# Optimization experiments

Hardware: AMD Instinct MI355X
Metric: run time of the kernel (lower is better)

The kernel has to match this reference:

```python
import jax, jax.numpy as jnp
import numpy as np

D_MODEL = 1024
N_HEADS = 16
HEAD_DIM = D_MODEL // N_HEADS


def setup_inputs() -> dict:
    key = jax.random.key(0)
    ks = jax.random.split(key, 9)
    s = 0.02
    x = jax.random.normal(ks[0], (2, 2048, D_MODEL), dtype=jnp.float32)
    wq = jax.random.normal(ks[1], (D_MODEL, D_MODEL), dtype=jnp.float32) * s
    wk = jax.random.normal(ks[2], (D_MODEL, D_MODEL), dtype=jnp.float32) * s
    wv = jax.random.normal(ks[3], (D_MODEL, D_MODEL), dtype=jnp.float32) * s
    wo = jax.random.normal(ks[4], (D_MODEL, D_MODEL), dtype=jnp.float32) * s
    bq = jax.random.normal(ks[5], (D_MODEL,), dtype=jnp.float32) * s
    bk = jax.random.normal(ks[6], (D_MODEL,), dtype=jnp.float32) * s
    bv = jax.random.normal(ks[7], (D_MODEL,), dtype=jnp.float32) * s
    bo = jax.random.normal(ks[8], (D_MODEL,), dtype=jnp.float32) * s
    return {"x": x, "wq": wq, "bq": bq, "wk": wk, "bk": bk,
            "wv": wv, "bv": bv, "wo": wo, "bo": bo}


def reference(x, wq, bq, wk, bk, wv, bv, wo, bo):
    B, T, C = x.shape
    H, Dh = N_HEADS, HEAD_DIM
    # torch Linear: y = x @ W.T + b
    q = (x @ wq.T + bq).reshape(B, T, H, Dh).transpose(0, 2, 1, 3)  # [B,H,T,Dh]
    k = (x @ wk.T + bk).reshape(B, T, H, Dh).transpose(0, 2, 1, 3)
    v = (x @ wv.T + bv).reshape(B, T, H, Dh).transpose(0, 2, 1, 3)
    scale = 1.0 / jnp.sqrt(jnp.float32(Dh))
    score = jnp.einsum('bhqd,bhkd->bhqk', q, k) * scale  # [B,H,T,T]
    causal = jnp.triu(jnp.ones((T, T), dtype=jnp.bool_), k=1)
    score = jnp.where(causal[None, None], jnp.float32(-10000.0), score)
    attn = jax.nn.softmax(score, axis=-1)
    out = jnp.einsum('bhqk,bhkd->bhqd', attn, v)  # [B,H,T,Dh]
    out = out.transpose(0, 2, 1, 3).reshape(B, T, C)
    return out @ wo.T + bo
```

## Files before the change

kernel.cpp:

```cpp
#include <hip/hip_runtime.h>
#include <hip/hip_bf16.h>

typedef __bf16 bf16_t;
typedef __bf16 bf16x8 __attribute__((ext_vector_type(8)));
typedef __bf16 bf16x4 __attribute__((ext_vector_type(4)));
typedef float f32x4 __attribute__((ext_vector_type(4)));
typedef unsigned int u32;

#define D_MODEL 1024
#define T_SEQ   2048
#define N_HEADS 16

#define WAITVM(N) asm volatile("s_waitcnt vmcnt(" #N ")" ::: "memory")

__device__ __forceinline__ void gload_lds16(const void* g, void* l) {
  __builtin_amdgcn_global_load_lds((const __attribute__((address_space(1))) u32*)g,
                                   (__attribute__((address_space(3))) u32*)l, 16, 0, 0);
}

__device__ __forceinline__ float fast_exp2(float x) {
#if __has_builtin(__builtin_amdgcn_exp2f)
  return __builtin_amdgcn_exp2f(x);
#else
  return __expf(x * 0.69314718056f);
#endif
}

struct CastArgs { const float* src[5]; bf16_t* dst[5]; };

__global__ __launch_bounds__(256) void cast_all(CastArgs p) {
  unsigned i = (blockIdx.x * 256u + threadIdx.x) * 4u;
  int seg; unsigned off;
  if (i < 4194304u) { seg = 0; off = i; }
  else { unsigned r = i - 4194304u; seg = 1 + (int)(r >> 20); off = r & 1048575u; }
  const float4 v = *(const float4*)(p.src[seg] + off);
  bf16x4 o = { (bf16_t)v.x, (bf16_t)v.y, (bf16_t)v.z, (bf16_t)v.w };
  *(bf16x4*)(p.dst[seg] + off) = o;
}

#define QSCL 0.18033688011112042f

struct QKVArgs {
  const bf16_t* A;
  const bf16_t* W[3];
  const float* bias[3];
  bf16_t* out[3];
};

__global__ __launch_bounds__(512, 2) void qkv_gemm(QKVArgs p) {
  __shared__ bf16_t lds[2 * 28672];

  const int tid = threadIdx.x;
  const int l = tid & 63, wid = tid >> 6;
  const int lh = l >> 4, r15 = l & 15;

  const int lid = blockIdx.x;
  const int bx = lid >> 4, by = lid & 15;
  const int brow = bx * 256;
  const int gcol0 = by * 192;

  const int wr = (wid >> 2) * 128;
  const int wc = (wid & 3) * 48;
  const int wrc = (wr >> 4);
  const int wcc = (wc >> 4);
  const int sA = (lh ^ ((r15 >> 1) & 3)) * 8;
  const int roff = r15 * 32;

  const int srow = l >> 2;
  const int gs = ((l & 3) ^ ((l >> 3) & 3)) * 8;

  f32x4 acc[8][3];
  const f32x4 zero = {0.f, 0.f, 0.f, 0.f};
#pragma unroll
  for (int i = 0; i < 8; ++i)
#pragma unroll
    for (int j = 0; j < 3; ++j) acc[i][j] = zero;

  const bf16_t* A = p.A;

  auto stageA = [&](bf16_t* buf, int k0, int kh) {
#pragma unroll
    for (int i = 0; i < 2; ++i) {
      int c = wid * 2 + i;
      gload_lds16(A + (size_t)(brow + c * 16 + srow) * D_MODEL + k0 + kh * 32 + gs,
                  buf + kh * 8192 + c * 512);
    }
  };
  auto stageB = [&](bf16_t* buf, int k0) {
#pragma unroll
    for (int i = 0; i < 3; ++i) {
      int g = wid * 3 + i;
      int kh = g >= 12;
      int c = g - kh * 12;
      int gcol = gcol0 + c * 16 + srow;
      int z = gcol >> 10;
      const bf16_t* w = (z == 0) ? p.W[0] : ((z == 1) ? p.W[1] : p.W[2]);
      gload_lds16(w + (size_t)(gcol & 1023) * D_MODEL + k0 + kh * 32 + gs,
                  buf + 16384 + kh * 6144 + c * 512);
    }
  };

  stageA(lds, 0, 0);
  stageA(lds, 0, 1);
  stageB(lds, 0);
  WAITVM(0);
  __builtin_amdgcn_s_barrier();

  for (int t = 0; t < 16; ++t) {
    bf16_t* cur = lds + (t & 1) * 28672;
    bf16_t* nxt = lds + ((t + 1) & 1) * 28672;
    const int k1 = (t + 1) * 64;
    const bool more = (t < 15);

    bf16x8 bfr[3][2];
#pragma unroll
    for (int ph = 0; ph < 4; ++ph) {
      bf16x8 a[2][2];
#pragma unroll
      for (int jj = 0; jj < 2; ++jj)
#pragma unroll
        for (int kh = 0; kh < 2; ++kh)
          a[jj][kh] = *(const bf16x8*)(cur + kh * 8192 + (wrc + 2 * ph + jj) * 512 + roff + sA);
      if (ph == 0) {
#pragma unroll
        for (int ni = 0; ni < 3; ++ni)
#pragma unroll
          for (int kh = 0; kh < 2; ++kh)
            bfr[ni][kh] = *(const bf16x8*)(cur + 16384 + kh * 6144 + (wcc + ni) * 512 + roff + sA);
      }
      if (more) {
        if (ph == 0) stageA(nxt, k1, 0);
        else if (ph == 1) stageA(nxt, k1, 1);
        else if (ph == 2) stageB(nxt, k1);
      }
      __builtin_amdgcn_s_barrier();
      __builtin_amdgcn_s_setprio(1);
#pragma unroll
      for (int jj = 0; jj < 2; ++jj)
#pragma unroll
        for (int ni = 0; ni < 3; ++ni) {
          acc[2 * ph + jj][ni] = __builtin_amdgcn_mfma_f32_16x16x32_bf16(a[jj][0], bfr[ni][0], acc[2 * ph + jj][ni], 0, 0, 0);
          acc[2 * ph + jj][ni] = __builtin_amdgcn_mfma_f32_16x16x32_bf16(a[jj][1], bfr[ni][1], acc[2 * ph + jj][ni], 0, 0, 0);
        }
      __builtin_amdgcn_s_setprio(0);
      if (ph == 3 && more) WAITVM(0);
      __builtin_amdgcn_s_barrier();
    }
  }

#pragma unroll
  for (int ni = 0; ni < 3; ++ni) {
    const int col = gcol0 + wc + ni * 16 + r15;
    const int z = col >> 10;
    const int zc = col & 1023;
    const float* bias = (z == 0) ? p.bias[0] : ((z == 1) ? p.bias[1] : p.bias[2]);
    bf16_t* O = (z == 0) ? p.out[0] : ((z == 1) ? p.out[1] : p.out[2]);
    const float bz = bias[zc];
    if (z == 2) {
#pragma unroll
      for (int mi = 0; mi < 8; ++mi) {
        int row0 = brow + wr + mi * 16 + lh * 4;
        int bb = row0 >> 11, t0 = row0 & 2047;
        bf16x4 pk;
#pragma unroll
        for (int j = 0; j < 4; ++j) pk[j] = (bf16_t)(acc[mi][ni][j] + bz);
        *(bf16x4*)(O + (size_t)bb * (D_MODEL * T_SEQ) + (size_t)zc * T_SEQ + t0) = pk;
      }
    } else if (z == 0) {
#pragma unroll
      for (int mi = 0; mi < 8; ++mi) {
        int row0 = brow + wr + mi * 16 + lh * 4;
#pragma unroll
        for (int j = 0; j < 4; ++j)
          O[(size_t)(row0 + j) * D_MODEL + zc] = (bf16_t)((acc[mi][ni][j] + bz) * QSCL);
      }
    } else {
#pragma unroll
      for (int mi = 0; mi < 8; ++mi) {
        int row0 = brow + wr + mi * 16 + lh * 4;
#pragma unroll
        for (int j = 0; j < 4; ++j)
          O[(size_t)(row0 + j) * D_MODEL + zc] = (bf16_t)(acc[mi][ni][j] + bz);
      }
    }
  }
}

__device__ __forceinline__ void stage_ab64(
    const bf16_t* __restrict__ A, const bf16_t* __restrict__ W,
    bf16_t* buf, int brow, int bcol, int k0, int w, int l) {
  const int srow = l >> 2;
  const int scol = ((l & 3) ^ ((l >> 3) & 3)) * 8;
#pragma unroll
  for (int i = 0; i < 3; ++i) {
    int ch = w * 3 + i;
    const bf16_t* src = (ch < 4)
      ? A + (size_t)(brow + ch * 16 + srow) * D_MODEL + k0 + scol
      : W + (size_t)(bcol + (ch - 4) * 16 + srow) * D_MODEL + k0 + scol;
    gload_lds16(src, buf + ch * 512);
  }
}

__device__ __forceinline__ void gemm_tile_64(
    const bf16_t* __restrict__ A, const bf16_t* __restrict__ W,
    bf16_t* bufs, int brow, int bcol, f32x4 acc[2][4])
{
  const int tid = threadIdx.x;
  const int l = tid & 63, w = tid >> 6;
  const int wr = (w >> 1) * 32, wc = (w & 1) * 64;
  const int lh = l >> 4, r15 = l & 15;
  const int NS = D_MODEL / 32;

  stage_ab64(A, W, bufs + 0 * 6144, brow, bcol, 0, w, l);
  stage_ab64(A, W, bufs + 1 * 6144, brow, bcol, 32, w, l);

  for (int t = 0; t < NS; ++t) {
    bf16_t* bb = bufs + (t % 3) * 6144;
    if (t + 2 < NS) {
      stage_ab64(A, W, bufs + ((t + 2) % 3) * 6144, brow, bcol, (t + 2) * 32, w, l);
      WAITVM(6);
    } else if (t + 1 < NS) {
      WAITVM(3);
    } else {
      WAITVM(0);
    }
    __builtin_amdgcn_s_barrier();

    bf16x8 af[2], bfr[4];
#pragma unroll
    for (int mi = 0; mi < 2; ++mi) {
      int rr = wr + mi * 16 + r15;
      int s = lh ^ ((rr >> 1) & 3);
      af[mi] = *(const bf16x8*)(bb + rr * 32 + s * 8);
    }
#pragma unroll
    for (int ni = 0; ni < 4; ++ni) {
      int rr = wc + ni * 16 + r15;
      int s = lh ^ ((rr >> 1) & 3);
      bfr[ni] = *(const bf16x8*)(bb + 2048 + rr * 32 + s * 8);
    }
    __builtin_amdgcn_s_setprio(1);
#pragma unroll
    for (int mi = 0; mi < 2; ++mi)
#pragma unroll
      for (int ni = 0; ni < 4; ++ni)
        acc[mi][ni] = __builtin_amdgcn_mfma_f32_16x16x32_bf16(af[mi], bfr[ni], acc[mi][ni], 0, 0, 0);
    __builtin_amdgcn_s_setprio(0);
    __builtin_amdgcn_s_barrier();
  }
}

__global__ __launch_bounds__(256) void out_gemm(
    const bf16_t* __restrict__ A, const bf16_t* __restrict__ W,
    const float* __restrict__ bias, float* __restrict__ O)
{
  __shared__ bf16_t bufs[3 * 6144];
  f32x4 acc[2][4];
  f32x4 zero = {0.f, 0.f, 0.f, 0.f};
#pragma unroll
  for (int i = 0; i < 2; ++i)
#pragma unroll
    for (int j = 0; j < 4; ++j) acc[i][j] = zero;

  const int brow = blockIdx.x * 64, bcol = blockIdx.y * 128;
  gemm_tile_64(A, W, bufs, brow, bcol, acc);

  const int tid = threadIdx.x, l = tid & 63, w = tid >> 6;
  const int wr = (w >> 1) * 32, wc = (w & 1) * 64, lh = l >> 4, r15 = l & 15;
#pragma unroll
  for (int ni = 0; ni < 4; ++ni) {
    int col = bcol + wc + ni * 16 + r15;
    float bz = bias[col];
#pragma unroll
    for (int mi = 0; mi < 2; ++mi) {
      int row0 = brow + wr + mi * 16 + lh * 4;
#pragma unroll
      for (int j = 0; j < 4; ++j)
        O[(size_t)(row0 + j) * D_MODEL + col] = acc[mi][ni][j] + bz;
    }
  }
}

__device__ __forceinline__ void stage_k128(const bf16_t* Kg, bf16_t* Kd, int kv0, int w, int l) {
#pragma unroll
  for (int i = 0; i < 4; ++i) {
    int c = w * 4 + i;
    int row = c * 8 + (l >> 3);
    int gcol = ((l & 7) ^ ((l >> 3) & 7)) * 8;
    gload_lds16(Kg + (size_t)(kv0 + row) * D_MODEL + gcol, Kd + c * 512);
  }
}
__device__ __forceinline__ void stage_v128(const bf16_t* Vg, bf16_t* Vd, int kv0, int w, int l) {
#pragma unroll
  for (int i = 0; i < 4; ++i) {
    int c = w * 4 + i;
    int drow = c * 4 + (l >> 4);
    int gkv = ((l & 15) ^ (drow & 15)) * 8;
    gload_lds16(Vg + (size_t)drow * T_SEQ + kv0 + gkv, Vd + c * 512);
  }
}

__global__ __launch_bounds__(256) void flash_attn(
    const bf16_t* __restrict__ Qm, const bf16_t* __restrict__ Km,
    const bf16_t* __restrict__ Vtg, bf16_t* __restrict__ Om)
{
  __shared__ bf16_t Kls[128 * 64];
  __shared__ bf16_t Vls[64 * 128];
  __shared__ bf16_t Pls[4][2][16 * 72];

  const int tid = threadIdx.x, l = tid & 63, w = tid >> 6;
  const int lh = l >> 4, r15 = l & 15;

  const int lid = blockIdx.x;
  const int qt = 31 - (lid >> 5);
  const int bh = lid & 31;
  const int b = bh >> 4, h = bh & 15;
  const int nT = (qt >> 1) + 1;

  const size_t baseQ = (size_t)b * T_SEQ * D_MODEL + h * 64;
  const size_t baseVt = (size_t)b * (D_MODEL * T_SEQ) + (size_t)(h * 64) * T_SEQ;
  const bf16_t* Kg = Km + baseQ;
  const bf16_t* Vg = Vtg + baseVt;

  const int qw = qt * 64 + w * 16;
  const int qrow = qw + r15;

  bf16x8 qf[2];
  {
    const bf16_t* qp = Qm + baseQ + (size_t)(qw + r15) * D_MODEL + lh * 8;
    qf[0] = *(const bf16x8*)(qp);
    qf[1] = *(const bf16x8*)(qp + 32);
  }

  float l_r = 0.f;
  f32x4 o_acc[4];
  const f32x4 zero = {0.f, 0.f, 0.f, 0.f};
#pragma unroll
  for (int n = 0; n < 4; ++n) o_acc[n] = zero;

  bf16_t* PA = &Pls[w][0][0];
  bf16_t* PB = &Pls[w][1][0];

  stage_k128(Kg, Kls, 0, w, l);
  stage_v128(Vg, Vls, 0, w, l);
  WAITVM(0);
  __builtin_amdgcn_s_barrier();

  for (int t = 0; t < nT; ++t) {
    const int kv0 = t * 128;
    const bool more = (t + 1 < nT);
    const bool diag = (t == nT - 1);
    const bool skip2 = diag && ((qt & 1) == 0);

    f32x4 sf[8];
    auto qk_n = [&](int n) {
      const int kvc = n * 16 + r15;
      const int sw = kvc & 7;
      bf16x8 kf0 = *(const bf16x8*)(Kls + kvc * 64 + ((lh ^ sw) * 8));
      bf16x8 kf1 = *(const bf16x8*)(Kls + kvc * 64 + (((4 + lh) ^ sw) * 8));
      f32x4 a = zero;
      a = __builtin_amdgcn_mfma_f32_16x16x32_bf16(kf0, qf[0], a, 0, 0, 0);
      a = __builtin_amdgcn_mfma_f32_16x16x32_bf16(kf1, qf[1], a, 0, 0, 0);
      sf[n] = a;
    };
    __builtin_amdgcn_s_setprio(1);
#pragma unroll
    for (int n = 0; n < 4; ++n) qk_n(n);
    __builtin_amdgcn_s_setprio(0);
    if (!skip2) {
      __builtin_amdgcn_s_setprio(1);
#pragma unroll
      for (int n = 4; n < 8; ++n) qk_n(n);
      __builtin_amdgcn_s_setprio(0);
    }

    __builtin_amdgcn_s_barrier();
    if (more) stage_k128(Kg, Kls, kv0 + 128, w, l);

    auto sm_half = [&](int hh, bf16_t* P, bool dm) {
#pragma unroll
      for (int n2 = 0; n2 < 4; ++n2) {
        const int n = hh * 4 + n2;
        float pv[4];
#pragma unroll
        for (int j = 0; j < 4; ++j) {
          float pp = fast_exp2(sf[n][j]);
          if (dm) {
            const int kvcol = kv0 + hh * 64 + n2 * 16 + lh * 4 + j;
            if (kvcol > qrow) pp = 0.f;
          }
          pv[j] = pp;
          l_r += pp;
        }
        bf16x4 pk = { (bf16_t)pv[0], (bf16_t)pv[1], (bf16_t)pv[2], (bf16_t)pv[3] };
        *(bf16x4*)(P + r15 * 72 + (n2 * 2 + (lh >> 1)) * 8 + (lh & 1) * 4) = pk;
      }
    };
    sm_half(0, PA, diag);
    if (!skip2) sm_half(1, PB, diag);

    if (more) WAITVM(4); else WAITVM(0);

    auto pv_half = [&](int hh, const bf16_t* P) {
      bf16x8 pa0 = *(const bf16x8*)(P + r15 * 72 + lh * 8);
      bf16x8 pa1 = *(const bf16x8*)(P + r15 * 72 + (4 + lh) * 8);
      __builtin_amdgcn_s_setprio(1);
#pragma unroll
      for (int nD = 0; nD < 4; ++nD) {
        const int d = nD * 16 + r15;
        const int b0 = (hh * 8 + lh) ^ r15;
        const int b1 = (hh * 8 + 4 + lh) ^ r15;
        bf16x8 vf0 = *(const bf16x8*)(Vls + d * 128 + b0 * 8);
        bf16x8 vf1 = *(const bf16x8*)(Vls + d * 128 + b1 * 8);
        o_acc[nD] = __builtin_amdgcn_mfma_f32_16x16x32_bf16(vf0, pa0, o_acc[nD], 0, 0, 0);
        o_acc[nD] = __builtin_amdgcn_mfma_f32_16x16x32_bf16(vf1, pa1, o_acc[nD], 0, 0, 0);
      }
      __builtin_amdgcn_s_setprio(0);
    };
    pv_half(0, PA);
    if (!skip2) pv_half(1, PB);

    __builtin_amdgcn_s_barrier();
    if (more) {
      stage_v128(Vg, Vls, kv0 + 128, w, l);
      WAITVM(4);
    }
  }

  float ls = l_r;
  ls += __shfl_xor(ls, 16, 64);
  ls += __shfl_xor(ls, 32, 64);
  const float invl = 1.f / ls;
  bf16_t* orow = Om + (size_t)(b * T_SEQ + qw + r15) * D_MODEL + h * 64;
#pragma unroll
  for (int n = 0; n < 4; ++n) {
    bf16x4 pk = { (bf16_t)(o_acc[n][0] * invl), (bf16_t)(o_acc[n][1] * invl),
                  (bf16_t)(o_acc[n][2] * invl), (bf16_t)(o_acc[n][3] * invl) };
    *(bf16x4*)(orow + n * 16 + lh * 4) = pk;
  }
}

extern "C" void kernel_launch(void* const* d_in, const int* in_sizes, int n_in,
                              void* d_out, int out_size, void* d_ws, size_t ws_size,
                              hipStream_t stream) {
  const float* x  = (const float*)d_in[0];
  const float* wq = (const float*)d_in[1];
  const float* bq = (const float*)d_in[2];
  const float* wk = (const float*)d_in[3];
  const float* bk = (const float*)d_in[4];
  const float* wv = (const float*)d_in[5];
  const float* bv = (const float*)d_in[6];
  const float* wo = (const float*)d_in[7];
  const float* bo = (const float*)d_in[8];

  char* ws = (char*)d_ws;
  const size_t MB = 1024 * 1024;
  bf16_t* xb  = (bf16_t*)(ws);
  bf16_t* wqb = (bf16_t*)(ws + 8 * MB);
  bf16_t* wkb = (bf16_t*)(ws + 10 * MB);
  bf16_t* wvb = (bf16_t*)(ws + 12 * MB);
  bf16_t* wob = (bf16_t*)(ws + 14 * MB);
  bf16_t* qb  = (bf16_t*)(ws + 16 * MB);
  bf16_t* kb  = (bf16_t*)(ws + 24 * MB);
  bf16_t* vtb = (bf16_t*)(ws + 32 * MB);
  bf16_t* ob  = (bf16_t*)(ws + 40 * MB);

  CastArgs ca;
  ca.src[0] = x;  ca.dst[0] = xb;
  ca.src[1] = wq; ca.dst[1] = wqb;
  ca.src[2] = wk; ca.dst[2] = wkb;
  ca.src[3] = wv; ca.dst[3] = wvb;
  ca.src[4] = wo; ca.dst[4] = wob;
  cast_all<<<8192, 256, 0, stream>>>(ca);

  QKVArgs qa;
  qa.A = xb;
  qa.W[0] = wqb; qa.W[1] = wkb; qa.W[2] = wvb;
  qa.bias[0] = bq; qa.bias[1] = bk; qa.bias[2] = bv;
  qa.out[0] = qb; qa.out[1] = kb; qa.out[2] = vtb;
  qkv_gemm<<<256, 512, 0, stream>>>(qa);

  flash_attn<<<1024, 256, 0, stream>>>(qb, kb, vtb, ob);

  out_gemm<<<dim3(64, 8), 256, 0, stream>>>(ob, wob, bo, (float*)d_out);
}
```

Baseline: 94.70 us.

## Split long causal attention query tiles across two blocks with combine kernel

Query tiles 16-31 (the longest causal rows) now have their KV range split in half across two blocks. A lookup table orders the 1536 blocks so that long work is scheduled first. Each split block writes an unnormalised fp32 partial output and row sum to a workspace, and a new combine kernel adds the two partials, normalises and writes bf16. This targets the load imbalance and tail of the causal flash-attention grid, at the cost of extra global traffic and one more kernel launch. Summing partials without a max rescale is only valid because the existing kernel already uses no running max.

```diff
diff --git a/kernel.cpp b/kernel.cpp
--- a/kernel.cpp
+++ b/kernel.cpp
@@ -281,6 +281,17 @@
   }
 }
 
+__device__ const unsigned char SCHED[48] = {
+  62, 94, 63, 95, 92, 93, 15, 14,
+  60, 61, 58, 90, 59, 91, 88, 89, 13, 12,
+  56, 57, 54, 86, 55, 87, 84, 85, 11, 10,
+  52, 53, 50, 82, 51, 83, 80, 81, 9, 8,
+  48, 49, 7, 6,
+  5, 4,
+  3, 2,
+  1, 0
+};
+
 __device__ __forceinline__ void stage_k128(const bf16_t* Kg, bf16_t* Kd, int kv0, int w, int l) {
 #pragma unroll
   for (int i = 0; i < 4; ++i) {
@@ -302,7 +313,8 @@
 
 __global__ __launch_bounds__(256) void flash_attn(
     const bf16_t* __restrict__ Qm, const bf16_t* __restrict__ Km,
-    const bf16_t* __restrict__ Vtg, bf16_t* __restrict__ Om)
+    const bf16_t* __restrict__ Vtg, bf16_t* __restrict__ Om,
+    float* __restrict__ Pw)
 {
   __shared__ bf16_t Kls[128 * 64];
   __shared__ bf16_t Vls[64 * 128];
@@ -312,10 +324,17 @@
   const int lh = l >> 4, r15 = l & 15;
 
   const int lid = blockIdx.x;
-  const int qt = 31 - (lid >> 5);
+  const int e = SCHED[lid >> 5];
+  const int qt = e & 31;
+  const int mode = e >> 5;
   const int bh = lid & 31;
   const int b = bh >> 4, h = bh & 15;
   const int nT = (qt >> 1) + 1;
+  const int h0 = nT >> 1;
+  const int t0 = (mode == 2) ? h0 : 0;
+  const int t1 = (mode == 1) ? h0 : nT;
+  const bool split = (mode != 0);
+  const int s = (mode == 2) ? 1 : 0;
 
   const size_t baseQ = (size_t)b * T_SEQ * D_MODEL + h * 64;
   const size_t baseVt = (size_t)b * (D_MODEL * T_SEQ) + (size_t)(h * 64) * T_SEQ;
@@ -341,14 +360,14 @@
   bf16_t* PA = &Pls[w][0][0];
   bf16_t* PB = &Pls[w][1][0];
 
-  stage_k128(Kg, Kls, 0, w, l);
-  stage_v128(Vg, Vls, 0, w, l);
+  stage_k128(Kg, Kls, t0 * 128, w, l);
+  stage_v128(Vg, Vls, t0 * 128, w, l);
   WAITVM(0);
   __builtin_amdgcn_s_barrier();
 
-  for (int t = 0; t < nT; ++t) {
+  for (int t = t0; t < t1; ++t) {
     const int kv0 = t * 128;
-    const bool more = (t + 1 < nT);
+    const bool more = (t + 1 < t1);
     const bool diag = (t == nT - 1);
     const bool skip2 = diag && ((qt & 1) == 0);
 
@@ -430,13 +449,48 @@
   float ls = l_r;
   ls += __shfl_xor(ls, 16, 64);
   ls += __shfl_xor(ls, 32, 64);
-  const float invl = 1.f / ls;
-  bf16_t* orow = Om + (size_t)(b * T_SEQ + qw + r15) * D_MODEL + h * 64;
-#pragma unroll
-  for (int n = 0; n < 4; ++n) {
-    bf16x4 pk = { (bf16_t)(o_acc[n][0] * invl), (bf16_t)(o_acc[n][1] * invl),
-                  (bf16_t)(o_acc[n][2] * invl), (bf16_t)(o_acc[n][3] * invl) };
-    *(bf16x4*)(orow + n * 16 + lh * 4) = pk;
+
+  if (!split) {
+    const float invl = 1.f / ls;
+    bf16_t* orow = Om + (size_t)(b * T_SEQ + qw + r15) * D_MODEL + h * 64;
+#pragma unroll
+    for (int n = 0; n < 4; ++n) {
+      bf16x4 pk = { (bf16_t)(o_acc[n][0] * invl), (bf16_t)(o_acc[n][1] * invl),
+                    (bf16_t)(o_acc[n][2] * invl), (bf16_t)(o_acc[n][3] * invl) };
+      *(bf16x4*)(orow + n * 16 + lh * 4) = pk;
+    }
+  } else {
+    float* slot = Pw + ((size_t)((qt - 16) * 32 + bh) * 2 + s) * 4160;
+    float* prow = slot + (w * 16 + r15) * 64;
+#pragma unroll
+    for (int n = 0; n < 4; ++n)
+      *(f32x4*)(prow + n * 16 + lh * 4) = o_acc[n];
+    if (lh == 0) slot[4096 + w * 16 + r15] = ls;
+  }
+}
+
+__global__ __launch_bounds__(256) void combine_attn(
+    const float* __restrict__ Pw, bf16_t* __restrict__ Om)
+{
+  const int g = blockIdx.x;
+  const int qt = 16 + (g >> 5);
+  const int bh = g & 31;
+  const int b = bh >> 4, h = bh & 15;
+  const int row = threadIdx.x >> 2;
+  const int cs = (threadIdx.x & 3) * 16;
+
+  const float* s0 = Pw + (size_t)((qt - 16) * 32 + bh) * 2 * 4160;
+  const float* s1 = s0 + 4160;
+  const float invl = 1.f / (s0[4096 + row] + s1[4096 + row]);
+
+  bf16_t* orow = Om + (size_t)(b * T_SEQ + qt * 64 + row) * D_MODEL + h * 64 + cs;
+#pragma unroll
+  for (int k4 = 0; k4 < 4; ++k4) {
+    float4 a = *(const float4*)(s0 + row * 64 + cs + k4 * 4);
+    float4 c = *(const float4*)(s1 + row * 64 + cs + k4 * 4);
+    bf16x4 pk = { (bf16_t)((a.x + c.x) * invl), (bf16_t)((a.y + c.y) * invl),
+                  (bf16_t)((a.z + c.z) * invl), (bf16_t)((a.w + c.w) * invl) };
+    *(bf16x4*)(orow + k4 * 4) = pk;
   }
 }
 
@@ -464,6 +518,7 @@
   bf16_t* kb  = (bf16_t*)(ws + 24 * MB);
   bf16_t* vtb = (bf16_t*)(ws + 32 * MB);
   bf16_t* ob  = (bf16_t*)(ws + 40 * MB);
+  float* pbuf = (float*)(ws + 64 * MB);
 
   CastArgs ca;
   ca.src[0] = x;  ca.dst[0] = xb;
@@ -480,7 +535,8 @@
   qa.out[0] = qb; qa.out[1] = kb; qa.out[2] = vtb;
   qkv_gemm<<<256, 512, 0, stream>>>(qa);
 
-  flash_attn<<<1024, 256, 0, stream>>>(qb, kb, vtb, ob);
+  flash_attn<<<1536, 256, 0, stream>>>(qb, kb, vtb, ob, pbuf);
+  combine_attn<<<512, 256, 0, stream>>>(pbuf, ob);
 
   out_gemm<<<dim3(64, 8), 256, 0, stream>>>(ob, wob, bo, (float*)d_out);
 }
```

Result: slower. 102.2 us (+7.9%).

## Process two 64-row query tiles per flash-attention block to reuse staged K/V

Applied to the files above, without the earlier changes.

Each block now handles 128 query rows: each warp owns two 16-row groups, A and B, and each staged 128-wide K/V tile serves both groups. This halves the grid to 512 blocks and the number of K/V loads into LDS per query row. Block order is also interleaved so heavy and light causal tiles mix. The cost is more registers (two accumulator sets), a serialized A-then-B dependency through the shared P buffers, and a full vmcnt(0) wait each iteration instead of the earlier partial wait, which may reduce overlap and occupancy.

```diff
diff --git a/kernel.cpp b/kernel.cpp
--- a/kernel.cpp
+++ b/kernel.cpp
@@ -312,31 +312,37 @@
   const int lh = l >> 4, r15 = l & 15;
 
   const int lid = blockIdx.x;
-  const int qt = 31 - (lid >> 5);
+  const int g = lid >> 5;
+  const int qt = (g < 8) ? (15 - g) : (g - 8);
   const int bh = lid & 31;
   const int b = bh >> 4, h = bh & 15;
-  const int nT = (qt >> 1) + 1;
+  const int nT = qt + 1;
 
   const size_t baseQ = (size_t)b * T_SEQ * D_MODEL + h * 64;
   const size_t baseVt = (size_t)b * (D_MODEL * T_SEQ) + (size_t)(h * 64) * T_SEQ;
   const bf16_t* Kg = Km + baseQ;
   const bf16_t* Vg = Vtg + baseVt;
 
-  const int qw = qt * 64 + w * 16;
-  const int qrow = qw + r15;
-
-  bf16x8 qf[2];
+  const int qA = qt * 128 + w * 16;
+  const int qB = qA + 64;
+  const int qrowA = qA + r15;
+  const int qrowB = qB + r15;
+
+  bf16x8 qfA[2], qfB[2];
   {
-    const bf16_t* qp = Qm + baseQ + (size_t)(qw + r15) * D_MODEL + lh * 8;
-    qf[0] = *(const bf16x8*)(qp);
-    qf[1] = *(const bf16x8*)(qp + 32);
-  }
-
-  float l_r = 0.f;
-  f32x4 o_acc[4];
+    const bf16_t* qp = Qm + baseQ + (size_t)qrowA * D_MODEL + lh * 8;
+    qfA[0] = *(const bf16x8*)(qp);
+    qfA[1] = *(const bf16x8*)(qp + 32);
+    const bf16_t* qp2 = Qm + baseQ + (size_t)qrowB * D_MODEL + lh * 8;
+    qfB[0] = *(const bf16x8*)(qp2);
+    qfB[1] = *(const bf16x8*)(qp2 + 32);
+  }
+
+  float l_A = 0.f, l_B = 0.f;
+  f32x4 oA[4], oB[4];
   const f32x4 zero = {0.f, 0.f, 0.f, 0.f};
 #pragma unroll
-  for (int n = 0; n < 4; ++n) o_acc[n] = zero;
+  for (int n = 0; n < 4; ++n) { oA[n] = zero; oB[n] = zero; }
 
   bf16_t* PA = &Pls[w][0][0];
   bf16_t* PB = &Pls[w][1][0];
@@ -349,11 +355,9 @@
   for (int t = 0; t < nT; ++t) {
     const int kv0 = t * 128;
     const bool more = (t + 1 < nT);
-    const bool diag = (t == nT - 1);
-    const bool skip2 = diag && ((qt & 1) == 0);
-
-    f32x4 sf[8];
-    auto qk_n = [&](int n) {
+    const bool last = (t == nT - 1);
+
+    auto qk_n = [&](const bf16x8* qf, int n, f32x4* sf) {
       const int kvc = n * 16 + r15;
       const int sw = kvc & 7;
       bf16x8 kf0 = *(const bf16x8*)(Kls + kvc * 64 + ((lh ^ sw) * 8));
@@ -363,21 +367,7 @@
       a = __builtin_amdgcn_mfma_f32_16x16x32_bf16(kf1, qf[1], a, 0, 0, 0);
       sf[n] = a;
     };
-    __builtin_amdgcn_s_setprio(1);
-#pragma unroll
-    for (int n = 0; n < 4; ++n) qk_n(n);
-    __builtin_amdgcn_s_setprio(0);
-    if (!skip2) {
-      __builtin_amdgcn_s_setprio(1);
-#pragma unroll
-      for (int n = 4; n < 8; ++n) qk_n(n);
-      __builtin_amdgcn_s_setprio(0);
-    }
-
-    __builtin_amdgcn_s_barrier();
-    if (more) stage_k128(Kg, Kls, kv0 + 128, w, l);
-
-    auto sm_half = [&](int hh, bf16_t* P, bool dm) {
+    auto sm_half = [&](const f32x4* sf, int hh, bf16_t* P, int qrow, bool dm, float& lr) {
 #pragma unroll
       for (int n2 = 0; n2 < 4; ++n2) {
         const int n = hh * 4 + n2;
@@ -390,18 +380,13 @@
             if (kvcol > qrow) pp = 0.f;
           }
           pv[j] = pp;
-          l_r += pp;
+          lr += pp;
         }
         bf16x4 pk = { (bf16_t)pv[0], (bf16_t)pv[1], (bf16_t)pv[2], (bf16_t)pv[3] };
         *(bf16x4*)(P + r15 * 72 + (n2 * 2 + (lh >> 1)) * 8 + (lh & 1) * 4) = pk;
       }
     };
-    sm_half(0, PA, diag);
-    if (!skip2) sm_half(1, PB, diag);
-
-    if (more) WAITVM(4); else WAITVM(0);
-
-    auto pv_half = [&](int hh, const bf16_t* P) {
+    auto pv_half = [&](int hh, const bf16_t* P, f32x4* o_acc) {
       bf16x8 pa0 = *(const bf16x8*)(P + r15 * 72 + lh * 8);
       bf16x8 pa1 = *(const bf16x8*)(P + r15 * 72 + (4 + lh) * 8);
       __builtin_amdgcn_s_setprio(1);
@@ -417,26 +402,72 @@
       }
       __builtin_amdgcn_s_setprio(0);
     };
-    pv_half(0, PA);
-    if (!skip2) pv_half(1, PB);
-
+
+    {
+      f32x4 sfA[8];
+      __builtin_amdgcn_s_setprio(1);
+#pragma unroll
+      for (int n = 0; n < 4; ++n) qk_n(qfA, n, sfA);
+      __builtin_amdgcn_s_setprio(0);
+      if (!last) {
+        __builtin_amdgcn_s_setprio(1);
+#pragma unroll
+        for (int n = 4; n < 8; ++n) qk_n(qfA, n, sfA);
+        __builtin_amdgcn_s_setprio(0);
+      }
+      sm_half(sfA, 0, PA, qrowA, last, l_A);
+      if (!last) sm_half(sfA, 1, PB, qrowA, false, l_A);
+    }
+
+    f32x4 sfB[8];
+    __builtin_amdgcn_s_setprio(1);
+#pragma unroll
+    for (int n = 0; n < 8; ++n) qk_n(qfB, n, sfB);
+    __builtin_amdgcn_s_setprio(0);
+
+    WAITVM(0);
     __builtin_amdgcn_s_barrier();
+    if (more) stage_k128(Kg, Kls, kv0 + 128, w, l);
+
+    pv_half(0, PA, oA);
+    if (!last) pv_half(1, PB, oA);
+    sm_half(sfB, 0, PA, qrowB, false, l_B);
+    sm_half(sfB, 1, PB, qrowB, last, l_B);
+    pv_half(0, PA, oB);
+    pv_half(1, PB, oB);
+
     if (more) {
+      WAITVM(0);
+      __builtin_amdgcn_s_barrier();
       stage_v128(Vg, Vls, kv0 + 128, w, l);
-      WAITVM(4);
-    }
-  }
-
-  float ls = l_r;
-  ls += __shfl_xor(ls, 16, 64);
-  ls += __shfl_xor(ls, 32, 64);
-  const float invl = 1.f / ls;
-  bf16_t* orow = Om + (size_t)(b * T_SEQ + qw + r15) * D_MODEL + h * 64;
-#pragma unroll
-  for (int n = 0; n < 4; ++n) {
-    bf16x4 pk = { (bf16_t)(o_acc[n][0] * invl), (bf16_t)(o_acc[n][1] * invl),
-                  (bf16_t)(o_acc[n][2] * invl), (bf16_t)(o_acc[n][3] * invl) };
-    *(bf16x4*)(orow + n * 16 + lh * 4) = pk;
+    }
+  }
+
+  {
+    float ls = l_A;
+    ls += __shfl_xor(ls, 16, 64);
+    ls += __shfl_xor(ls, 32, 64);
+    const float invl = 1.f / ls;
+    bf16_t* orow = Om + (size_t)(b * T_SEQ + qrowA) * D_MODEL + h * 64;
+#pragma unroll
+    for (int n = 0; n < 4; ++n) {
+      bf16x4 pk = { (bf16_t)(oA[n][0] * invl), (bf16_t)(oA[n][1] * invl),
+                    (bf16_t)(oA[n][2] * invl), (bf16_t)(oA[n][3] * invl) };
+      *(bf16x4*)(orow + n * 16 + lh * 4) = pk;
+    }
+  }
+  {
+    float ls = l_B;
+    ls += __shfl_xor(ls, 16, 64);
+    ls += __shfl_xor(ls, 32, 64);
+    const float invl = 1.f / ls;
+    bf16_t* orow = Om + (size_t)(b * T_SEQ + qrowB) * D_MODEL + h * 64;
+#pragma unroll
+    for (int n = 0; n < 4; ++n) {
+      bf16x4 pk = { (bf16_t)(oB[n][0] * invl), (bf16_t)(oB[n][1] * invl),
+                    (bf16_t)(oB[n][2] * invl), (bf16_t)(oB[n][3] * invl) };
+      *(bf16x4*)(orow + n * 16 + lh * 4) = pk;
+    }
   }
 }
 
@@ -480,7 +511,7 @@
   qa.out[0] = qb; qa.out[1] = kb; qa.out[2] = vtb;
   qkv_gemm<<<256, 512, 0, stream>>>(qa);
 
-  flash_attn<<<1024, 256, 0, stream>>>(qb, kb, vtb, ob);
+  flash_attn<<<512, 256, 0, stream>>>(qb, kb, vtb, ob);
 
   out_gemm<<<dim3(64, 8), 256, 0, stream>>>(ob, wob, bo, (float*)d_out);
 }
```

After: 101.1 us. 6.7% more time.

## Restructure attention P buffer with XOR swizzle and regroup GEMM staging

Applied to the files above, without the earlier changes.

In the GEMM kernel, all three next-tile stage loads are now issued in phase 0 instead of spread over phases 0-2. In flash attention, the per-wave P buffer is cut to a single 16x64 tile with an XOR swizzle instead of padding, and softmax and PV are interleaved per half. Wait counts become full drains before each barrier. The aim is less LDS use and fewer bank conflicts, at the cost of less overlap between global loads and compute because of the full vmcnt(0) waits.

```diff
diff --git a/kernel.cpp b/kernel.cpp
--- a/kernel.cpp
+++ b/kernel.cpp
@@ -127,11 +127,11 @@
 #pragma unroll
           for (int kh = 0; kh < 2; ++kh)
             bfr[ni][kh] = *(const bf16x8*)(cur + 16384 + kh * 6144 + (wcc + ni) * 512 + roff + sA);
-      }
-      if (more) {
-        if (ph == 0) stageA(nxt, k1, 0);
-        else if (ph == 1) stageA(nxt, k1, 1);
-        else if (ph == 2) stageB(nxt, k1);
+        if (more) {
+          stageA(nxt, k1, 0);
+          stageA(nxt, k1, 1);
+          stageB(nxt, k1);
+        }
       }
       __builtin_amdgcn_s_barrier();
       __builtin_amdgcn_s_setprio(1);
@@ -306,7 +306,7 @@
 {
   __shared__ bf16_t Kls[128 * 64];
   __shared__ bf16_t Vls[64 * 128];
-  __shared__ bf16_t Pls[4][2][16 * 72];
+  __shared__ bf16_t Pls[4][16 * 64];
 
   const int tid = threadIdx.x, l = tid & 63, w = tid >> 6;
   const int lh = l >> 4, r15 = l & 15;
@@ -324,10 +324,11 @@
 
   const int qw = qt * 64 + w * 16;
   const int qrow = qw + r15;
+  const int sw7 = r15 & 7;
 
   bf16x8 qf[2];
   {
-    const bf16_t* qp = Qm + baseQ + (size_t)(qw + r15) * D_MODEL + lh * 8;
+    const bf16_t* qp = Qm + baseQ + (size_t)qrow * D_MODEL + lh * 8;
     qf[0] = *(const bf16x8*)(qp);
     qf[1] = *(const bf16x8*)(qp + 32);
   }
@@ -338,8 +339,7 @@
 #pragma unroll
   for (int n = 0; n < 4; ++n) o_acc[n] = zero;
 
-  bf16_t* PA = &Pls[w][0][0];
-  bf16_t* PB = &Pls[w][1][0];
+  bf16_t* P = &Pls[w][0];
 
   stage_k128(Kg, Kls, 0, w, l);
   stage_v128(Vg, Vls, 0, w, l);
@@ -374,10 +374,11 @@
       __builtin_amdgcn_s_setprio(0);
     }
 
+    WAITVM(0);
     __builtin_amdgcn_s_barrier();
     if (more) stage_k128(Kg, Kls, kv0 + 128, w, l);
 
-    auto sm_half = [&](int hh, bf16_t* P, bool dm) {
+    auto sm_half = [&](int hh, bool dm) {
 #pragma unroll
       for (int n2 = 0; n2 < 4; ++n2) {
         const int n = hh * 4 + n2;
@@ -393,17 +394,13 @@
           l_r += pp;
         }
         bf16x4 pk = { (bf16_t)pv[0], (bf16_t)pv[1], (bf16_t)pv[2], (bf16_t)pv[3] };
-        *(bf16x4*)(P + r15 * 72 + (n2 * 2 + (lh >> 1)) * 8 + (lh & 1) * 4) = pk;
+        const int slot = n2 * 2 + (lh >> 1);
+        *(bf16x4*)(P + r15 * 64 + ((slot ^ sw7) * 8) + (lh & 1) * 4) = pk;
       }
     };
-    sm_half(0, PA, diag);
-    if (!skip2) sm_half(1, PB, diag);
-
-    if (more) WAITVM(4); else WAITVM(0);
-
-    auto pv_half = [&](int hh, const bf16_t* P) {
-      bf16x8 pa0 = *(const bf16x8*)(P + r15 * 72 + lh * 8);
-      bf16x8 pa1 = *(const bf16x8*)(P + r15 * 72 + (4 + lh) * 8);
+    auto pv_half = [&](int hh) {
+      bf16x8 pa0 = *(const bf16x8*)(P + r15 * 64 + ((lh ^ sw7) * 8));
+      bf16x8 pa1 = *(const bf16x8*)(P + r15 * 64 + (((4 + lh) ^ sw7) * 8));
       __builtin_amdgcn_s_setprio(1);
 #pragma unroll
       for (int nD = 0; nD < 4; ++nD) {
@@ -417,21 +414,24 @@
       }
       __builtin_amdgcn_s_setprio(0);
     };
-    pv_half(0, PA);
-    if (!skip2) pv_half(1, PB);
-
+
+    sm_half(0, diag);
+    pv_half(0);
+    if (!skip2) {
+      sm_half(1, diag);
+      pv_half(1);
+    }
+
+    WAITVM(0);
     __builtin_amdgcn_s_barrier();
-    if (more) {
-      stage_v128(Vg, Vls, kv0 + 128, w, l);
-      WAITVM(4);
-    }
+    if (more) stage_v128(Vg, Vls, kv0 + 128, w, l);
   }
 
   float ls = l_r;
   ls += __shfl_xor(ls, 16, 64);
   ls += __shfl_xor(ls, 32, 64);
   const float invl = 1.f / ls;
-  bf16_t* orow = Om + (size_t)(b * T_SEQ + qw + r15) * D_MODEL + h * 64;
+  bf16_t* orow = Om + (size_t)(b * T_SEQ + qrow) * D_MODEL + h * 64;
 #pragma unroll
   for (int n = 0; n < 4; ++n) {
     bf16x4 pk = { (bf16_t)(o_acc[n][0] * invl), (bf16_t)(o_acc[n][1] * invl),
```

New measurement: 97.99 us. 3.5% more time.
